# Optimization experiments

Hardware: AMD Instinct MI355X
Metric: run time of the kernel (lower is better)

Reference implementation:

```python
import jax, jax.numpy as jnp
import numpy as np
import math

L, B, E, H = 1024, 16, 512, 8
NUM_REL = 2 * L - 1  # 2047


def setup_inputs() -> dict:
    key = jax.random.key(0)
    ks = jax.random.split(key, 9)
    s = 0.02
    query = jax.random.normal(ks[0], (L, B, E), dtype=jnp.float32)
    return {
        "query": query,
        "key": jax.random.normal(ks[1], (L, B, E), dtype=jnp.float32),
        "value": jax.random.normal(ks[2], (L, B, E), dtype=jnp.float32),
        "in_proj_weight": jax.random.normal(ks[3], (3 * E, E), dtype=jnp.float32) * s,
        "in_proj_bias": jax.random.normal(ks[4], (3 * E,), dtype=jnp.float32) * s,
        "out_proj_weight": jax.random.normal(ks[5], (E, E), dtype=jnp.float32) * s,
        "out_proj_bias": jax.random.normal(ks[6], (E,), dtype=jnp.float32) * s,
        "rpe_weight_table": jax.random.normal(ks[7], (H, NUM_REL), dtype=jnp.float32) * s,
        "rpe_indices": jax.random.randint(ks[8], (L, L), 0, NUM_REL, dtype=jnp.int32),
    }


def _heads(x, w, b):
    # x: (N, Bn, E), w: (E, E), b: (E,) -> (Bn, H, N, d)
    n, bn, e = x.shape
    d = e // H
    y = jnp.einsum('nbe,fe->nbf', x, w) + b
    return y.reshape(n, bn, H, d).transpose(1, 2, 0, 3)


def reference(query, key, value, in_proj_weight, in_proj_bias, out_proj_weight,
              out_proj_bias, rpe_weight_table, rpe_indices):
    l, bn, e = query.shape
    d = e // H
    wq, wk, wv = jnp.split(in_proj_weight, 3, axis=0)
    bq, bk, bv = jnp.split(in_proj_bias, 3, axis=0)
    q = _heads(query, wq, bq)   # (B, H, L, d)
    k = _heads(key, wk, bk)     # (B, H, S, d)
    v = _heads(value, wv, bv)   # (B, H, S, d)
    q = q / math.sqrt(d)
    # rel-pos bias: gather table -> (H, L, S), broadcast over batch
    bias = rpe_weight_table[:, rpe_indices]
    attn = jnp.einsum('bhld,bhsd->bhls', q, k) + bias[None]
    attn = jax.nn.softmax(attn, axis=-1)
    out = jnp.einsum('bhls,bhsd->bhld', attn, v)   # (B, H, L, d)
    out = out.transpose(2, 0, 1, 3).reshape(l, bn, e)  # (L, B, E)
    out = jnp.einsum('lbe,fe->lbf', out, out_proj_weight) + out_proj_bias
    return out
```

## Files before the change

### kernel.cpp

```cpp
#include <hip/hip_runtime.h>
#include <hip/hip_bf16.h>


#define L_SEQ 1024
#define B_N   16
#define E_DIM 512
#define H_N   8
#define NREL  2047

typedef _Float16 f16;
using half8   = __attribute__((ext_vector_type(8))) _Float16;
using floatx4 = __attribute__((ext_vector_type(4))) float;

__device__ __forceinline__ half8 cvt8(const float4 a, const float4 b) {
    half8 h;
    h[0] = (f16)a.x; h[1] = (f16)a.y; h[2] = (f16)a.z; h[3] = (f16)a.w;
    h[4] = (f16)b.x; h[5] = (f16)b.y; h[6] = (f16)b.z; h[7] = (f16)b.w;
    return h;
}

__global__ __launch_bounds__(256) void qkv_kernel(
    const float* __restrict__ Xq, const float* __restrict__ Xk, const float* __restrict__ Xv,
    const float* __restrict__ W, const float* __restrict__ Bias,
    f16* __restrict__ Qo, f16* __restrict__ Ko, f16* __restrict__ Vo)
{
    const int flat = blockIdx.x;
    const int xcd  = flat & 7;
    const int slot = flat >> 3;
    const int g    = xcd * 48 + (slot >> 2);
    const int f0   = (slot & 3) << 7;
    const int proj = g >> 7;
    const int n0   = (g & 127) << 7;

    const float* X  = (proj == 0) ? Xq : (proj == 1) ? Xk : Xv;
    const float* Wp = W + (size_t)(proj << 9) * E_DIM;

    __shared__ __align__(16) f16 As[128][40];
    __shared__ __align__(16) f16 Bs[128][40];

    const int tid  = threadIdx.x;
    const int w    = tid >> 6;
    const int lane = tid & 63;
    const int quad = lane >> 4, c = lane & 15;
    const int wm = (w >> 1) << 6, wn = (w & 1) << 6;

    const int srow = tid >> 1;
    const int sseg = (tid & 1) << 4;

    const float* xrow = X  + (size_t)(n0 + srow) * E_DIM + sseg;
    const float* wrow = Wp + (size_t)(f0 + srow) * E_DIM + sseg;

    floatx4 acc[4][4] = {};

    float4 px0 = *reinterpret_cast<const float4*>(xrow);
    float4 px1 = *reinterpret_cast<const float4*>(xrow + 4);
    float4 px2 = *reinterpret_cast<const float4*>(xrow + 8);
    float4 px3 = *reinterpret_cast<const float4*>(xrow + 12);
    float4 pw0 = *reinterpret_cast<const float4*>(wrow);
    float4 pw1 = *reinterpret_cast<const float4*>(wrow + 4);
    float4 pw2 = *reinterpret_cast<const float4*>(wrow + 8);
    float4 pw3 = *reinterpret_cast<const float4*>(wrow + 12);

    for (int k0 = 0; k0 < E_DIM; k0 += 32) {
        __syncthreads();
        *reinterpret_cast<half8*>(&As[srow][sseg])     = cvt8(px0, px1);
        *reinterpret_cast<half8*>(&As[srow][sseg + 8]) = cvt8(px2, px3);
        *reinterpret_cast<half8*>(&Bs[srow][sseg])     = cvt8(pw0, pw1);
        *reinterpret_cast<half8*>(&Bs[srow][sseg + 8]) = cvt8(pw2, pw3);
        __syncthreads();

        if (k0 + 32 < E_DIM) {
            const float* xn = xrow + k0 + 32;
            const float* wn2 = wrow + k0 + 32;
            px0 = *reinterpret_cast<const float4*>(xn);
            px1 = *reinterpret_cast<const float4*>(xn + 4);
            px2 = *reinterpret_cast<const float4*>(xn + 8);
            px3 = *reinterpret_cast<const float4*>(xn + 12);
            pw0 = *reinterpret_cast<const float4*>(wn2);
            pw1 = *reinterpret_cast<const float4*>(wn2 + 4);
            pw2 = *reinterpret_cast<const float4*>(wn2 + 8);
            pw3 = *reinterpret_cast<const float4*>(wn2 + 12);
        }

        half8 a[4], bfr[4];
#pragma unroll
        for (int mt = 0; mt < 4; ++mt)
            a[mt] = *reinterpret_cast<const half8*>(&As[wm + mt * 16 + c][quad * 8]);
#pragma unroll
        for (int nt = 0; nt < 4; ++nt)
            bfr[nt] = *reinterpret_cast<const half8*>(&Bs[wn + nt * 16 + c][quad * 8]);
#pragma unroll
        for (int mt = 0; mt < 4; ++mt)
#pragma unroll
            for (int nt = 0; nt < 4; ++nt)
                acc[mt][nt] = __builtin_amdgcn_mfma_f32_16x16x32_f16(a[mt], bfr[nt], acc[mt][nt], 0, 0, 0);
    }

    f16* Dst = (proj == 0) ? Qo : (proj == 1) ? Ko : Vo;
    const float scale = (proj == 0) ? 0.125f : 1.0f;

#pragma unroll
    for (int nt = 0; nt < 4; ++nt) {
        const int fl = f0 + wn + nt * 16 + c;
        const float bj = Bias[(proj << 9) + fl];
        const int h = fl >> 6, d = fl & 63;
#pragma unroll
        for (int mt = 0; mt < 4; ++mt) {
#pragma unroll
            for (int r = 0; r < 4; ++r) {
                const int n = n0 + wm + mt * 16 + quad * 4 + r;
                const int l = n >> 4, b = n & 15;
                Dst[((((size_t)b * H_N + h) * L_SEQ + l) << 6) + d] =
                    (f16)((acc[mt][nt][r] + bj) * scale);
            }
        }
    }
}

__global__ __launch_bounds__(256) void transpose_v(
    const f16* __restrict__ V, f16* __restrict__ Vt)
{
    const int l0 = blockIdx.x << 6;
    const size_t base = (size_t)blockIdx.y << 16;
    __shared__ __align__(16) f16 T[64][72];
    const int tid = threadIdx.x;
    const int r = tid >> 2, co = (tid & 3) << 4;

    const uint4 a0 = *reinterpret_cast<const uint4*>(V + base + (size_t)(l0 + r) * 64 + co);
    const uint4 a1 = *reinterpret_cast<const uint4*>(V + base + (size_t)(l0 + r) * 64 + co + 8);
    *reinterpret_cast<uint4*>(&T[r][co])     = a0;
    *reinterpret_cast<uint4*>(&T[r][co + 8]) = a1;
    __syncthreads();

    union { f16 h[16]; uint4 u[2]; } pk;
#pragma unroll
    for (int j = 0; j < 16; ++j) pk.h[j] = T[co + j][r];
    *reinterpret_cast<uint4*>(Vt + base + (size_t)r * 1024 + l0 + co)     = pk.u[0];
    *reinterpret_cast<uint4*>(Vt + base + (size_t)r * 1024 + l0 + co + 8) = pk.u[1];
}

__global__ __launch_bounds__(256, 3) void attn_kernel(
    const f16* __restrict__ Q, const f16* __restrict__ K, const f16* __restrict__ Vt,
    const int* __restrict__ RPE, const float* __restrict__ Tab, f16* __restrict__ CTX)
{
    const int q0 = blockIdx.x << 7;
    const int bh = blockIdx.y;
    const int b = bh >> 3, h = bh & 7;

    const int tid  = threadIdx.x;
    const int w    = tid >> 6;
    const int lane = tid & 63;
    const int quad = lane >> 4, c = lane & 15;

    __shared__ __align__(16) f16 Ks[64][72];
    __shared__ __align__(16) f16 Vts[64][72];
    __shared__ __align__(16) f16 Pw[4][32][72];
    __shared__ float tab[NREL];

    const size_t base = (size_t)bh << 16;

    for (int i = tid; i < NREL; i += 256) tab[i] = Tab[h * NREL + i];

    const int qg0 = q0 + (w << 5);
    half8 Aq[2][2];
#pragma unroll
    for (int s = 0; s < 2; ++s) {
        const f16* qp = Q + base + (size_t)(qg0 + s * 16 + c) * 64 + quad * 8;
        Aq[s][0] = *reinterpret_cast<const half8*>(qp);
        Aq[s][1] = *reinterpret_cast<const half8*>(qp + 32);
    }

    floatx4 o[2][4] = {};
    float l_part[2][4] = {};

    const int* rp = RPE + (size_t)(qg0 + (quad << 2)) * 1024 + c;

    const int sr = tid >> 2, so = (tid & 3) << 4;
    const f16* kbase = K  + base + (size_t)sr * 64 + so;
    const f16* vbase = Vt + base + (size_t)sr * 1024 + so;

    uint4 pk0 = *reinterpret_cast<const uint4*>(kbase);
    uint4 pk1 = *reinterpret_cast<const uint4*>(kbase + 8);
    uint4 pv0 = *reinterpret_cast<const uint4*>(vbase);
    uint4 pv1 = *reinterpret_cast<const uint4*>(vbase + 8);

    for (int j0 = 0; j0 < L_SEQ; j0 += 64) {
        __syncthreads();
        *reinterpret_cast<uint4*>(&Ks[sr][so])      = pk0;
        *reinterpret_cast<uint4*>(&Ks[sr][so + 8])  = pk1;
        *reinterpret_cast<uint4*>(&Vts[sr][so])     = pv0;
        *reinterpret_cast<uint4*>(&Vts[sr][so + 8]) = pv1;
        __syncthreads();

        if (j0 + 64 < L_SEQ) {
            const f16* kn = kbase + (size_t)(j0 + 64) * 64;
            const f16* vn = vbase + (j0 + 64);
            pk0 = *reinterpret_cast<const uint4*>(kn);
            pk1 = *reinterpret_cast<const uint4*>(kn + 8);
            pv0 = *reinterpret_cast<const uint4*>(vn);
            pv1 = *reinterpret_cast<const uint4*>(vn + 8);
        }

        int idx[2][4][4];
#pragma unroll
        for (int s = 0; s < 2; ++s)
#pragma unroll
            for (int r = 0; r < 4; ++r)
#pragma unroll
                for (int nt = 0; nt < 4; ++nt)
                    idx[s][r][nt] = rp[(size_t)(s * 16 + r) * 1024 + j0 + nt * 16];

        floatx4 sc[2][4];
#pragma unroll
        for (int nt = 0; nt < 4; ++nt) {
            const half8 b0 = *reinterpret_cast<const half8*>(&Ks[nt * 16 + c][quad * 8]);
            const half8 b1 = *reinterpret_cast<const half8*>(&Ks[nt * 16 + c][32 + quad * 8]);
            floatx4 t0 = {}, t1 = {};
            t0 = __builtin_amdgcn_mfma_f32_16x16x32_f16(Aq[0][0], b0, t0, 0, 0, 0);
            t0 = __builtin_amdgcn_mfma_f32_16x16x32_f16(Aq[0][1], b1, t0, 0, 0, 0);
            t1 = __builtin_amdgcn_mfma_f32_16x16x32_f16(Aq[1][0], b0, t1, 0, 0, 0);
            t1 = __builtin_amdgcn_mfma_f32_16x16x32_f16(Aq[1][1], b1, t1, 0, 0, 0);
            sc[0][nt] = t0; sc[1][nt] = t1;
        }

#pragma unroll
        for (int s = 0; s < 2; ++s)
#pragma unroll
            for (int r = 0; r < 4; ++r) {
                float rs = 0.0f;
#pragma unroll
                for (int nt = 0; nt < 4; ++nt) {
                    const float p = __expf(sc[s][nt][r] + tab[idx[s][r][nt]]);
                    rs += p;
                    Pw[w][s * 16 + quad * 4 + r][nt * 16 + c] = (f16)p;
                }
                l_part[s][r] += rs;
            }

        half8 vb[4][2];
#pragma unroll
        for (int nt = 0; nt < 4; ++nt) {
            vb[nt][0] = *reinterpret_cast<const half8*>(&Vts[nt * 16 + c][quad * 8]);
            vb[nt][1] = *reinterpret_cast<const half8*>(&Vts[nt * 16 + c][32 + quad * 8]);
        }
#pragma unroll
        for (int s = 0; s < 2; ++s) {
            const half8 Ap0 = *reinterpret_cast<const half8*>(&Pw[w][s * 16 + c][quad * 8]);
            const half8 Ap1 = *reinterpret_cast<const half8*>(&Pw[w][s * 16 + c][32 + quad * 8]);
#pragma unroll
            for (int nt = 0; nt < 4; ++nt) {
                o[s][nt] = __builtin_amdgcn_mfma_f32_16x16x32_f16(Ap0, vb[nt][0], o[s][nt], 0, 0, 0);
                o[s][nt] = __builtin_amdgcn_mfma_f32_16x16x32_f16(Ap1, vb[nt][1], o[s][nt], 0, 0, 0);
            }
        }
    }

#pragma unroll
    for (int s = 0; s < 2; ++s)
#pragma unroll
        for (int r = 0; r < 4; ++r) {
            float l = l_part[s][r];
            l += __shfl_xor(l, 1); l += __shfl_xor(l, 2);
            l += __shfl_xor(l, 4); l += __shfl_xor(l, 8);
            const float inv = 1.0f / l;
            const int lrow = qg0 + s * 16 + quad * 4 + r;
            f16* dp = CTX + ((size_t)(lrow * 16 + b)) * 512 + h * 64;
#pragma unroll
            for (int nt = 0; nt < 4; ++nt)
                dp[nt * 16 + c] = (f16)(o[s][nt][r] * inv);
        }
}

__global__ __launch_bounds__(256) void out_kernel(
    const f16* __restrict__ X, const float* __restrict__ W, const float* __restrict__ Bias,
    float* __restrict__ Out)
{
    const int flat = blockIdx.x;
    const int xcd  = flat & 7;
    const int slot = flat >> 3;
    const int m    = xcd * 16 + (slot >> 2);
    const int f0   = (slot & 3) << 7;
    const int n0   = m << 7;

    __shared__ __align__(16) f16 As[128][40];
    __shared__ __align__(16) f16 Bs[128][40];

    const int tid  = threadIdx.x;
    const int w    = tid >> 6;
    const int lane = tid & 63;
    const int quad = lane >> 4, c = lane & 15;
    const int wm = (w >> 1) << 6, wn = (w & 1) << 6;

    const int srow = tid >> 1;
    const int sseg = (tid & 1) << 4;

    const f16*   xrow = X + (size_t)(n0 + srow) * E_DIM + sseg;
    const float* wrow = W + (size_t)(f0 + srow) * E_DIM + sseg;

    floatx4 acc[4][4] = {};

    uint4  pxu0 = *reinterpret_cast<const uint4*>(xrow);
    uint4  pxu1 = *reinterpret_cast<const uint4*>(xrow + 8);
    float4 pw0  = *reinterpret_cast<const float4*>(wrow);
    float4 pw1  = *reinterpret_cast<const float4*>(wrow + 4);
    float4 pw2  = *reinterpret_cast<const float4*>(wrow + 8);
    float4 pw3  = *reinterpret_cast<const float4*>(wrow + 12);

    for (int k0 = 0; k0 < E_DIM; k0 += 32) {
        __syncthreads();
        *reinterpret_cast<uint4*>(&As[srow][sseg])     = pxu0;
        *reinterpret_cast<uint4*>(&As[srow][sseg + 8]) = pxu1;
        *reinterpret_cast<half8*>(&Bs[srow][sseg])     = cvt8(pw0, pw1);
        *reinterpret_cast<half8*>(&Bs[srow][sseg + 8]) = cvt8(pw2, pw3);
        __syncthreads();

        if (k0 + 32 < E_DIM) {
            const f16*   xn = xrow + k0 + 32;
            const float* wn2 = wrow + k0 + 32;
            pxu0 = *reinterpret_cast<const uint4*>(xn);
            pxu1 = *reinterpret_cast<const uint4*>(xn + 8);
            pw0  = *reinterpret_cast<const float4*>(wn2);
            pw1  = *reinterpret_cast<const float4*>(wn2 + 4);
            pw2  = *reinterpret_cast<const float4*>(wn2 + 8);
            pw3  = *reinterpret_cast<const float4*>(wn2 + 12);
        }

        half8 a[4], bfr[4];
#pragma unroll
        for (int mt = 0; mt < 4; ++mt)
            a[mt] = *reinterpret_cast<const half8*>(&As[wm + mt * 16 + c][quad * 8]);
#pragma unroll
        for (int nt = 0; nt < 4; ++nt)
            bfr[nt] = *reinterpret_cast<const half8*>(&Bs[wn + nt * 16 + c][quad * 8]);
#pragma unroll
        for (int mt = 0; mt < 4; ++mt)
#pragma unroll
            for (int nt = 0; nt < 4; ++nt)
                acc[mt][nt] = __builtin_amdgcn_mfma_f32_16x16x32_f16(a[mt], bfr[nt], acc[mt][nt], 0, 0, 0);
    }

#pragma unroll
    for (int nt = 0; nt < 4; ++nt) {
        const int f = f0 + wn + nt * 16 + c;
        const float bj = Bias[f];
#pragma unroll
        for (int mt = 0; mt < 4; ++mt) {
#pragma unroll
            for (int r = 0; r < 4; ++r) {
                const int n = n0 + wm + mt * 16 + quad * 4 + r;
                Out[(size_t)n * E_DIM + f] = acc[mt][nt][r] + bj;
            }
        }
    }
}

extern "C" void kernel_launch(void* const* d_in, const int* in_sizes, int n_in,
                              void* d_out, int out_size, void* d_ws, size_t ws_size,
                              hipStream_t stream) {
    const float* q_in = (const float*)d_in[0];
    const float* k_in = (const float*)d_in[1];
    const float* v_in = (const float*)d_in[2];
    const float* ipw  = (const float*)d_in[3];
    const float* ipb  = (const float*)d_in[4];
    const float* opw  = (const float*)d_in[5];
    const float* opb  = (const float*)d_in[6];
    const float* tab  = (const float*)d_in[7];
    const int*   rpe  = (const int*)d_in[8];
    float* out = (float*)d_out;

    f16* ws   = (f16*)d_ws;
    f16* Q    = ws;
    f16* K    = ws + 8388608;
    f16* Vt   = ws + 16777216;
    f16* Vtmp = ws + 25165824;
    f16* CTX  = ws + 25165824;

    qkv_kernel<<<dim3(1536), 256, 0, stream>>>(q_in, k_in, v_in, ipw, ipb, Q, K, Vtmp);
    transpose_v<<<dim3(16, 128), 256, 0, stream>>>(Vtmp, Vt);
    attn_kernel<<<dim3(8, 128), 256, 0, stream>>>(Q, K, Vt, rpe, tab, CTX);
    out_kernel<<<dim3(512), 256, 0, stream>>>(CTX, opw, opb, out);
}
```

Measured before the change: 321.8 us.

## Stage projection GEMM tiles via direct global-to-LDS loads with XOR swizzle

Both projection GEMM kernels (QKV and output) stop staging through registers. They now use global_load_lds 16-byte transfers straight into shared memory, with an XOR-swizzled layout to avoid bank conflicts. Inputs stay fp32 in LDS and are converted to fp16 after the LDS read, before the MFMA. The register prefetch that overlapped the next tile's load with compute is removed, so each k-step now waits on its own load at the barrier. LDS footprint per block also doubles for the fp32 tiles.

```diff
diff --git a/kernel.cpp b/kernel.cpp
--- a/kernel.cpp
+++ b/kernel.cpp
@@ -17,6 +17,13 @@
     h[0] = (f16)a.x; h[1] = (f16)a.y; h[2] = (f16)a.z; h[3] = (f16)a.w;
     h[4] = (f16)b.x; h[5] = (f16)b.y; h[6] = (f16)b.z; h[7] = (f16)b.w;
     return h;
+}
+
+__device__ __forceinline__ void gl_lds16(const void* g, void* l) {
+    __builtin_amdgcn_global_load_lds(
+        (const __attribute__((address_space(1))) unsigned int*)g,
+        (__attribute__((address_space(3))) unsigned int*)l,
+        16, 0, 0);
 }
 
 __global__ __launch_bounds__(256) void qkv_kernel(
@@ -35,8 +42,8 @@
     const float* X  = (proj == 0) ? Xq : (proj == 1) ? Xk : Xv;
     const float* Wp = W + (size_t)(proj << 9) * E_DIM;
 
-    __shared__ __align__(16) f16 As[128][40];
-    __shared__ __align__(16) f16 Bs[128][40];
+    __shared__ __align__(16) float As[128 * 32];
+    __shared__ __align__(16) float Bs[128 * 32];
 
     const int tid  = threadIdx.x;
     const int w    = tid >> 6;
@@ -44,51 +51,40 @@
     const int quad = lane >> 4, c = lane & 15;
     const int wm = (w >> 1) << 6, wn = (w & 1) << 6;
 
-    const int srow = tid >> 1;
-    const int sseg = (tid & 1) << 4;
-
-    const float* xrow = X  + (size_t)(n0 + srow) * E_DIM + sseg;
-    const float* wrow = Wp + (size_t)(f0 + srow) * E_DIM + sseg;
+    const int lr = lane >> 3;
+    const int lc = (lane & 7) ^ lr;
+    const float* Xg = X  + (size_t)(n0 + (w << 3) + lr) * E_DIM + (lc << 2);
+    const float* Wg = Wp + (size_t)(f0 + (w << 3) + lr) * E_DIM + (lc << 2);
+
+    const int sa0 = (((quad << 1) ^ (c & 7)) << 2);
+    const int sa1 = sa0 ^ 4;
 
     floatx4 acc[4][4] = {};
 
-    float4 px0 = *reinterpret_cast<const float4*>(xrow);
-    float4 px1 = *reinterpret_cast<const float4*>(xrow + 4);
-    float4 px2 = *reinterpret_cast<const float4*>(xrow + 8);
-    float4 px3 = *reinterpret_cast<const float4*>(xrow + 12);
-    float4 pw0 = *reinterpret_cast<const float4*>(wrow);
-    float4 pw1 = *reinterpret_cast<const float4*>(wrow + 4);
-    float4 pw2 = *reinterpret_cast<const float4*>(wrow + 8);
-    float4 pw3 = *reinterpret_cast<const float4*>(wrow + 12);
-
     for (int k0 = 0; k0 < E_DIM; k0 += 32) {
         __syncthreads();
-        *reinterpret_cast<half8*>(&As[srow][sseg])     = cvt8(px0, px1);
-        *reinterpret_cast<half8*>(&As[srow][sseg + 8]) = cvt8(px2, px3);
-        *reinterpret_cast<half8*>(&Bs[srow][sseg])     = cvt8(pw0, pw1);
-        *reinterpret_cast<half8*>(&Bs[srow][sseg + 8]) = cvt8(pw2, pw3);
-        __syncthreads();
-
-        if (k0 + 32 < E_DIM) {
-            const float* xn = xrow + k0 + 32;
-            const float* wn2 = wrow + k0 + 32;
-            px0 = *reinterpret_cast<const float4*>(xn);
-            px1 = *reinterpret_cast<const float4*>(xn + 4);
-            px2 = *reinterpret_cast<const float4*>(xn + 8);
-            px3 = *reinterpret_cast<const float4*>(xn + 12);
-            pw0 = *reinterpret_cast<const float4*>(wn2);
-            pw1 = *reinterpret_cast<const float4*>(wn2 + 4);
-            pw2 = *reinterpret_cast<const float4*>(wn2 + 8);
-            pw3 = *reinterpret_cast<const float4*>(wn2 + 12);
-        }
+#pragma unroll
+        for (int i = 0; i < 4; ++i) {
+            gl_lds16(Xg + (size_t)i * (32 * E_DIM) + k0, &As[((i << 5) + (w << 3)) << 5]);
+            gl_lds16(Wg + (size_t)i * (32 * E_DIM) + k0, &Bs[((i << 5) + (w << 3)) << 5]);
+        }
+        __syncthreads();
 
         half8 a[4], bfr[4];
 #pragma unroll
-        for (int mt = 0; mt < 4; ++mt)
-            a[mt] = *reinterpret_cast<const half8*>(&As[wm + mt * 16 + c][quad * 8]);
-#pragma unroll
-        for (int nt = 0; nt < 4; ++nt)
-            bfr[nt] = *reinterpret_cast<const half8*>(&Bs[wn + nt * 16 + c][quad * 8]);
+        for (int mt = 0; mt < 4; ++mt) {
+            const int r = (wm + mt * 16 + c) << 5;
+            const float4 lo = *reinterpret_cast<const float4*>(&As[r + sa0]);
+            const float4 hi = *reinterpret_cast<const float4*>(&As[r + sa1]);
+            a[mt] = cvt8(lo, hi);
+        }
+#pragma unroll
+        for (int nt = 0; nt < 4; ++nt) {
+            const int r = (wn + nt * 16 + c) << 5;
+            const float4 lo = *reinterpret_cast<const float4*>(&Bs[r + sa0]);
+            const float4 hi = *reinterpret_cast<const float4*>(&Bs[r + sa1]);
+            bfr[nt] = cvt8(lo, hi);
+        }
 #pragma unroll
         for (int mt = 0; mt < 4; ++mt)
 #pragma unroll
@@ -282,8 +278,8 @@
     const int f0   = (slot & 3) << 7;
     const int n0   = m << 7;
 
-    __shared__ __align__(16) f16 As[128][40];
-    __shared__ __align__(16) f16 Bs[128][40];
+    __shared__ __align__(16) f16   As[128 * 32];
+    __shared__ __align__(16) float Bs[128 * 32];
 
     const int tid  = threadIdx.x;
     const int w    = tid >> 6;
@@ -291,47 +287,43 @@
     const int quad = lane >> 4, c = lane & 15;
     const int wm = (w >> 1) << 6, wn = (w & 1) << 6;
 
-    const int srow = tid >> 1;
-    const int sseg = (tid & 1) << 4;
-
-    const f16*   xrow = X + (size_t)(n0 + srow) * E_DIM + sseg;
-    const float* wrow = W + (size_t)(f0 + srow) * E_DIM + sseg;
+    const int ar  = lane >> 2;
+    const int ac  = (lane & 3) ^ ((lane >> 3) & 3);
+    const f16* Xg = X + (size_t)(n0 + (w << 4) + ar) * E_DIM + (ac << 3);
+
+    const int lr = lane >> 3;
+    const int lc = (lane & 7) ^ lr;
+    const float* Wg = W + (size_t)(f0 + (w << 3) + lr) * E_DIM + (lc << 2);
+
+    const int sa = ((quad ^ ((c >> 1) & 3)) << 3);
+    const int sb0 = (((quad << 1) ^ (c & 7)) << 2);
+    const int sb1 = sb0 ^ 4;
 
     floatx4 acc[4][4] = {};
 
-    uint4  pxu0 = *reinterpret_cast<const uint4*>(xrow);
-    uint4  pxu1 = *reinterpret_cast<const uint4*>(xrow + 8);
-    float4 pw0  = *reinterpret_cast<const float4*>(wrow);
-    float4 pw1  = *reinterpret_cast<const float4*>(wrow + 4);
-    float4 pw2  = *reinterpret_cast<const float4*>(wrow + 8);
-    float4 pw3  = *reinterpret_cast<const float4*>(wrow + 12);
-
     for (int k0 = 0; k0 < E_DIM; k0 += 32) {
         __syncthreads();
-        *reinterpret_cast<uint4*>(&As[srow][sseg])     = pxu0;
-        *reinterpret_cast<uint4*>(&As[srow][sseg + 8]) = pxu1;
-        *reinterpret_cast<half8*>(&Bs[srow][sseg])     = cvt8(pw0, pw1);
-        *reinterpret_cast<half8*>(&Bs[srow][sseg + 8]) = cvt8(pw2, pw3);
-        __syncthreads();
-
-        if (k0 + 32 < E_DIM) {
-            const f16*   xn = xrow + k0 + 32;
-            const float* wn2 = wrow + k0 + 32;
-            pxu0 = *reinterpret_cast<const uint4*>(xn);
-            pxu1 = *reinterpret_cast<const uint4*>(xn + 8);
-            pw0  = *reinterpret_cast<const float4*>(wn2);
-            pw1  = *reinterpret_cast<const float4*>(wn2 + 4);
-            pw2  = *reinterpret_cast<const float4*>(wn2 + 8);
-            pw3  = *reinterpret_cast<const float4*>(wn2 + 12);
-        }
+#pragma unroll
+        for (int i = 0; i < 2; ++i)
+            gl_lds16(Xg + (size_t)i * (64 * E_DIM) + k0, &As[((i << 6) + (w << 4)) << 5]);
+#pragma unroll
+        for (int i = 0; i < 4; ++i)
+            gl_lds16(Wg + (size_t)i * (32 * E_DIM) + k0, &Bs[((i << 5) + (w << 3)) << 5]);
+        __syncthreads();
 
         half8 a[4], bfr[4];
 #pragma unroll
-        for (int mt = 0; mt < 4; ++mt)
-            a[mt] = *reinterpret_cast<const half8*>(&As[wm + mt * 16 + c][quad * 8]);
-#pragma unroll
-        for (int nt = 0; nt < 4; ++nt)
-            bfr[nt] = *reinterpret_cast<const half8*>(&Bs[wn + nt * 16 + c][quad * 8]);
+        for (int mt = 0; mt < 4; ++mt) {
+            const int r = (wm + mt * 16 + c) << 5;
+            a[mt] = *reinterpret_cast<const half8*>(&As[r + sa]);
+        }
+#pragma unroll
+        for (int nt = 0; nt < 4; ++nt) {
+            const int r = (wn + nt * 16 + c) << 5;
+            const float4 lo = *reinterpret_cast<const float4*>(&Bs[r + sb0]);
+            const float4 hi = *reinterpret_cast<const float4*>(&Bs[r + sb1]);
+            bfr[nt] = cvt8(lo, hi);
+        }
 #pragma unroll
         for (int mt = 0; mt < 4; ++mt)
 #pragma unroll
```

New measurement: 320.4 us. Within noise of the previous version (-0.4%).
